# Kernel tuning notes

Measured on AMD Instinct MI355X. Metric: run time of the kernel, lower is better.

## Reference

```python
import jax, jax.numpy as jnp
import numpy as np

R, D = 8192, 128                  # rays, MPI depth planes (steps per ray)
NX, NY, NZ = 160, 160, 128        # world_size (NZ == mpi_depth)
PDIM, K0, WID, PE = 16, 12, 128, 4
RGBFEA = 4 * (9 + 3 + 3 + 3) + 6  # 78, rgbnet output dim
VSR = 256.0 / D                   # voxel_size_ratio (alpha interval)
LAM = 0.01                        # glob_lambda_den / glob_lambda_rgb


def _act_shift():
    # exact replication of the act_shift buffer init in __init__
    g = np.full([D], 1.0 / D - 1e-6)
    p = [1.0 - g[0]]
    for i in range(1, D):
        p.append((1.0 - g[:i + 1].sum()) / (1.0 - g[:i].sum()))
    p = np.asarray(p)
    return jnp.asarray(np.log(p ** (-1.0 / VSR) - 1.0) - 1.0, dtype=jnp.float32)


def setup_inputs() -> dict:
    key = jax.random.key(0)
    ks = jax.random.split(key, 8)
    dim0 = 3 + 3 * PE * 2 + K0  # 39
    return {
        "rays_o": jax.random.uniform(ks[0], (R, 3), jnp.float32),
        "rays_d": jax.random.normal(ks[1], (R, 3), jnp.float32),
        "density_grid": jax.random.normal(ks[2], (1, NX, NY, NZ), jnp.float32) * 0.1,
        "density_params_grid": jax.random.normal(ks[3], (PDIM, NX, NY, NZ), jnp.float32) * 0.05,
        "k0_grid": jax.random.normal(ks[4], (K0, NX, NY, NZ), jnp.float32) * 0.1,
        "global_flow_den": jnp.zeros((2,), jnp.float32),
        "global_flow_rgb": jnp.zeros((6,), jnp.float32),
        "w0": jax.random.normal(ks[5], (dim0, WID), jnp.float32) / np.sqrt(dim0),
        "b0": jnp.zeros((WID,), jnp.float32),
        "w1": jax.random.normal(ks[6], (WID, WID), jnp.float32) / np.sqrt(WID),
        "b1": jnp.zeros((WID,), jnp.float32),
        "w2": jax.random.normal(ks[7], (WID, RGBFEA), jnp.float32) / np.sqrt(WID),
        "b2": jnp.zeros((RGBFEA,), jnp.float32),
        "act_shift": _act_shift(),  # non-trainable buffer, shape [D]
    }


def _trilinear(grid, pts):
    # grid: [C, X, Y, Z]; pts: [N, 3] in [0, 1] -> returns [N, C]
    sizes_i = np.array(grid.shape[1:], dtype=np.int32)
    sizes_f = jnp.asarray(sizes_i, dtype=pts.dtype)
    g = jnp.clip(pts, 0.0, 1.0) * (sizes_f - 1.0)
    i0 = jnp.clip(jnp.floor(g).astype(jnp.int32), 0, jnp.asarray(sizes_i - 2))
    f = g - i0.astype(pts.dtype)
    out = jnp.zeros((grid.shape[0], pts.shape[0]), dtype=pts.dtype)
    for dx in (0, 1):
        wx = f[:, 0] if dx else 1.0 - f[:, 0]
        for dy in (0, 1):
            wy = f[:, 1] if dy else 1.0 - f[:, 1]
            for dz in (0, 1):
                wz = f[:, 2] if dz else 1.0 - f[:, 2]
                v = grid[:, i0[:, 0] + dx, i0[:, 1] + dy, i0[:, 2] + dz]  # [C, N] gather
                out = out + v * (wx * wy * wz)[None, :]
    return out.T


def reference(rays_o, rays_d, density_grid, density_params_grid, k0_grid,
              global_flow_den, global_flow_rgb, w0, b0, w1, b1, w2, b2, act_shift):
    # --- packed ray sampling over MPI depth planes (create_full_step_id pattern) ---
    t = jnp.linspace(0.0, 1.0, D, dtype=rays_o.dtype)
    pts = rays_o[:, None, :] + rays_d[:, None, :] * t[None, :, None]   # [R, D, 3]
    pts = jnp.clip(pts, 0.0, 1.0).reshape(-1, 3)                        # [R*D, 3]
    ray_id = jnp.repeat(jnp.arange(R, dtype=jnp.int32), D)              # [R*D]
    step_id = jnp.tile(jnp.arange(D, dtype=jnp.int32), R)               # [R*D]

    # --- grid trilinear sampling ---
    density = _trilinear(density_grid, pts)[:, 0]          # [N]
    params = _trilinear(density_params_grid, pts)          # [N, 16]
    k0f = _trilinear(k0_grid, pts)                          # [N, 12]

    # --- per-point normalizing-flow reparam on density (4 flow steps, 4 params each) ---
    z = density + global_flow_den[0] * LAM
    for i in range(4):
        p = params[:, 4 * i:4 * i + 4]
        z = z + p[:, 0] * jnp.tanh(p[:, 1] * z + p[:, 2]) * jax.nn.sigmoid(p[:, 3])

    # --- alpha from shifted density: 1 - exp(-softplus(den + shift) * interval) ---
    den = z + act_shift[step_id]
    alpha = 1.0 - jnp.exp(-jax.nn.softplus(den) * VSR)      # [N]

    # --- per-ray transmittance via exclusive cumprod ---
    a = alpha.reshape(R, D)
    T = jnp.cumprod(1.0 - a + 1e-10, axis=1)
    T_excl = jnp.concatenate([jnp.ones((R, 1), a.dtype), T[:, :-1]], axis=1)
    weights = a * T_excl                                     # [R, D]
    alphainv_last = T[:, -1]                                 # [R]

    # --- view-direction positional encoding, broadcast per point via ray_id gather ---
    viewdirs = rays_d / (jnp.linalg.norm(rays_d, axis=-1, keepdims=True) + 1e-8)
    freq = jnp.asarray([2.0 ** i for i in range(PE)], dtype=rays_d.dtype)
    ang = viewdirs[:, :, None] * freq[None, None, :]          # [R, 3, PE]
    emb = jnp.concatenate([viewdirs, jnp.sin(ang).reshape(R, -1), jnp.cos(ang).reshape(R, -1)], -1)  # [R, 27]

    # --- MLP shading ---
    h = jnp.concatenate([emb[ray_id], k0f], axis=-1)          # [N, 39]
    h = jax.nn.relu(h @ w0 + b0)
    h = jax.nn.relu(h @ w1 + b1)
    feat = h @ w2 + b2                                        # [N, 78]
    rgb = jax.nn.sigmoid(feat[:, :3] + global_flow_rgb[:3] * LAM)  # [N, 3]

    # --- segment-sum compositing over packed ray_id (white background) ---
    wflat = weights.reshape(-1)
    rgb_marched = jax.ops.segment_sum(wflat[:, None] * rgb, ray_id, num_segments=R)
    rgb_marched = rgb_marched + alphainv_last[:, None]
    return rgb_marched
```

## Files before the change

kernel.cpp:

```cpp
#include <hip/hip_runtime.h>
#include <math.h>

#define R_    8192
#define D_    128
#define RD    (R_ * D_)
#define NXg   160
#define NYg   160
#define NZg   128
#define CSg   (NXg * NYg * NZg)
#define WIDm  128
#define K0C   12
#define LAMc  0.01f
#define VSRc  2.0f

#define W1F_N   16384
#define W0KF_N  2048
#define W2F_N   4096
#define WTAB_N  (W1F_N + W0KF_N + W2F_N)
#define LW1     0
#define LW0K    W1F_N
#define LW2     (W1F_N + W0KF_N)

typedef __attribute__((ext_vector_type(8)))  short   short8v;
typedef __attribute__((ext_vector_type(4)))  float   f32x4;
typedef __attribute__((ext_vector_type(16))) float   f32x16;
typedef __attribute__((ext_vector_type(2)))  int     int2v;
typedef __attribute__((ext_vector_type(4)))  int     int4v;
typedef __attribute__((ext_vector_type(4)))  unsigned short ushort4v;
typedef __attribute__((ext_vector_type(8)))  unsigned short ushort8v;

static __device__ __forceinline__ unsigned short f2b(float f) {
    union { float f; unsigned int u; } v; v.f = f;
    unsigned int r = v.u + 0x7fffu + ((v.u >> 16) & 1u);
    return (unsigned short)(r >> 16);
}
static __device__ __forceinline__ float b2f(unsigned short u) {
    union { unsigned int u; float f; } v; v.u = ((unsigned int)u) << 16;
    return v.f;
}
static __device__ __forceinline__ unsigned int pk2(float lo, float hi) {
    unsigned int r;
    asm("v_cvt_pk_bf16_f32 %0, %1, %2" : "=v"(r) : "v"(lo), "v"(hi));
    return r;
}
static __device__ __forceinline__ short8v as_s8(int4v v) {
    union { int4v i; short8v s; } u; u.i = v; return u.s;
}

__global__ __launch_bounds__(256) void k_pack_t(
    const float* __restrict__ dg, const float* __restrict__ pg,
    const float* __restrict__ kg, unsigned short* __restrict__ vox)
{
    const int tid = threadIdx.x;
    const int g   = tid & 3;
    const int s2  = tid >> 2;
    const float* pl[8];
    bool padq[8];
#pragma unroll
    for (int q = 0; q < 8; ++q) {
        int ch = 8 * g + q;
        padq[q] = (ch >= 29);
        pl[q] = (ch == 0) ? dg
              : (ch < 17) ? pg + (size_t)(ch - 1) * CSg
              : (ch < 29) ? kg + (size_t)(ch - 17) * CSg
              : dg;
    }
#pragma unroll
    for (int it = 0; it < 4; ++it) {
        int vofs = (blockIdx.x * 4 + it) * 256 + 4 * s2;
        f32x4 L[8];
#pragma unroll
        for (int q = 0; q < 8; ++q) {
            f32x4 v = __builtin_nontemporal_load((const f32x4*)(pl[q] + vofs));
            if (padq[q]) v = f32x4{0.0f, 0.0f, 0.0f, 0.0f};
            L[q] = v;
        }
#pragma unroll
        for (int k = 0; k < 4; ++k) {
            int4v chunk;
#pragma unroll
            for (int h2 = 0; h2 < 4; ++h2)
                chunk[h2] = (int)pk2(L[2 * h2][k], L[2 * h2 + 1][k]);
            *(int4v*)((char*)vox + (size_t)(vofs + k) * 64 + g * 16) = chunk;
        }
    }
}

__global__ void k_prep_e(const float* __restrict__ rays_d,
                         const float* __restrict__ w0, const float* __restrict__ b0,
                         float* __restrict__ e) {
    int r = blockIdx.x;
    int j = threadIdx.x;
    float d0 = rays_d[r * 3 + 0], d1 = rays_d[r * 3 + 1], d2 = rays_d[r * 3 + 2];
    float nrm = sqrtf(d0 * d0 + d1 * d1 + d2 * d2) + 1e-8f;
    float v[3] = { d0 / nrm, d1 / nrm, d2 / nrm };
    float x[27];
    x[0] = v[0]; x[1] = v[1]; x[2] = v[2];
#pragma unroll
    for (int c = 0; c < 3; ++c)
#pragma unroll
        for (int f = 0; f < 4; ++f) {
            float ang = v[c] * (float)(1 << f);
            x[3 + c * 4 + f]  = sinf(ang);
            x[15 + c * 4 + f] = cosf(ang);
        }
    float acc = b0[j];
#pragma unroll
    for (int m = 0; m < 27; ++m) acc = fmaf(x[m], w0[m * WIDm + j], acc);
    e[r * WIDm + j] = acc;
}

__global__ void k_prep_frags32(const float* __restrict__ w0, const float* __restrict__ w1,
                               const float* __restrict__ w2,
                               unsigned short* __restrict__ wtab) {
    int t = blockIdx.x * 256 + threadIdx.x;
    if (t < W1F_N) {
        int tile = t >> 9, l = (t >> 3) & 63, j = t & 7;
        int mt = tile >> 3, ks = tile & 7;
        int m = mt * 32 + (l & 31);
        int k = ks * 16 + 8 * (l >> 5) + j;
        wtab[LW1 + t] = f2b(w1[k * WIDm + m]);
    } else if (t < W1F_N + W0KF_N) {
        int u = t - W1F_N;
        int mt = u >> 9, l = (u >> 3) & 63, j = u & 7;
        int m = mt * 32 + (l & 31);
        int k = 8 * (l >> 5) + j;
        wtab[LW0K + u] = f2b(k < K0C ? w0[(27 + k) * WIDm + m] : 0.0f);
    } else {
        int u = t - W1F_N - W0KF_N;
        int ks = u >> 9, l = (u >> 3) & 63, j = u & 7;
        int m = l & 31;
        int k = ks * 16 + 8 * (l >> 5) + j;
        wtab[LW2 + u] = f2b(m < 3 ? w2[k * 78 + m] : 0.0f);
    }
}

static __device__ __forceinline__ void finish_sample(
    int sid, int s, const float* acc , const float* __restrict__ gfd,
    const float* __restrict__ act_shift,
    float* __restrict__ alpha_ws, unsigned short* __restrict__ k0b)
{
    float z = acc[0] + gfd[0] * LAMc;
#pragma unroll
    for (int i = 0; i < 4; ++i) {
        float pa = acc[1 + 4 * i + 0], pb = acc[1 + 4 * i + 1];
        float pc = acc[1 + 4 * i + 2], pd = acc[1 + 4 * i + 3];
        float sg = 1.0f / (1.0f + expf(-pd));
        z += pa * tanhf(pb * z + pc) * sg;
    }
    float den = z + act_shift[s];
    float sp = fmaxf(den, 0.0f) + log1pf(expf(-fabsf(den)));
    alpha_ws[sid] = 1.0f - expf(-sp * VSRc);

    ushort8v lo, hi;
#pragma unroll
    for (int c = 0; c < 8; ++c) lo[c] = f2b(acc[17 + c]);
#pragma unroll
    for (int c = 0; c < 8; ++c) hi[c] = (c < 4) ? f2b(acc[17 + 8 + c]) : (unsigned short)0;
    *(ushort8v*)(k0b + (size_t)sid * 16)     = lo;
    *(ushort8v*)(k0b + (size_t)sid * 16 + 8) = hi;
}

static __device__ __forceinline__ void sample_coords(
    int sid, const float* __restrict__ rays_o, const float* __restrict__ rays_d,
    int& ix, int& iy, int& iz, float& fx, float& fy, float& fz)
{
    int r = sid >> 7;
    int s = sid & 127;
    float t = s * (1.0f / 127.0f);
    float px = fminf(fmaxf(rays_o[r * 3 + 0] + rays_d[r * 3 + 0] * t, 0.0f), 1.0f);
    float py = fminf(fmaxf(rays_o[r * 3 + 1] + rays_d[r * 3 + 1] * t, 0.0f), 1.0f);
    float pz = fminf(fmaxf(rays_o[r * 3 + 2] + rays_d[r * 3 + 2] * t, 0.0f), 1.0f);
    float gx = px * (float)(NXg - 1);
    float gy = py * (float)(NYg - 1);
    float gz = pz * (float)(NZg - 1);
    ix = min((int)gx, NXg - 2);
    iy = min((int)gy, NYg - 2);
    iz = min((int)gz, NZg - 2);
    fx = gx - (float)ix;
    fy = gy - (float)iy;
    fz = gz - (float)iz;
}

__global__ __launch_bounds__(256) void k_gather_aos(
    const float* __restrict__ rays_o, const float* __restrict__ rays_d,
    const unsigned short* __restrict__ vox,
    const float* __restrict__ gfd, const float* __restrict__ act_shift,
    float* __restrict__ alpha_ws, unsigned short* __restrict__ k0b)
{
    int sid = blockIdx.x * 256 + threadIdx.x;
    if (sid >= RD) return;
    int ix, iy, iz; float fx, fy, fz;
    sample_coords(sid, rays_o, rays_d, ix, iy, iz, fx, fy, fz);

    const unsigned short* base = vox + ((size_t)(ix * NYg + iy) * NZg + iz) * 32;
    const size_t qoff[4] = { 0, (size_t)NZg * 32, (size_t)NYg * NZg * 32,
                             (size_t)(NYg + 1) * NZg * 32 };
    float wxy[4];
    wxy[0] = (1.0f - fx) * (1.0f - fy);
    wxy[1] = (1.0f - fx) * fy;
    wxy[2] = fx * (1.0f - fy);
    wxy[3] = fx * fy;
    float wz0 = 1.0f - fz, wz1 = fz;

    float acc[29];
#pragma unroll
    for (int c = 0; c < 29; ++c) acc[c] = 0.0f;

#pragma unroll
    for (int q = 0; q < 4; ++q) {
        const unsigned short* p = base + qoff[q];
#pragma unroll
        for (int dz = 0; dz < 2; ++dz) {
            float w = wxy[q] * (dz ? wz1 : wz0);
            const ushort8v* pv = (const ushort8v*)(p + dz * 32);
            ushort8v v0 = pv[0], v1 = pv[1], v2 = pv[2], v3 = pv[3];
#pragma unroll
            for (int i = 0; i < 8; ++i) acc[i]      = fmaf(w, b2f(v0[i]), acc[i]);
#pragma unroll
            for (int i = 0; i < 8; ++i) acc[8 + i]  = fmaf(w, b2f(v1[i]), acc[8 + i]);
#pragma unroll
            for (int i = 0; i < 8; ++i) acc[16 + i] = fmaf(w, b2f(v2[i]), acc[16 + i]);
#pragma unroll
            for (int i = 0; i < 5; ++i) acc[24 + i] = fmaf(w, b2f(v3[i]), acc[24 + i]);
        }
    }
    finish_sample(sid, sid & 127, acc, gfd, act_shift, alpha_ws, k0b);
}

__global__ void k_gather_soa(
    const float* __restrict__ rays_o, const float* __restrict__ rays_d,
    const float* __restrict__ dg,  const float* __restrict__ pg,
    const float* __restrict__ kg,  const float* __restrict__ gfd,
    const float* __restrict__ act_shift,
    float* __restrict__ alpha_ws, unsigned short* __restrict__ k0b)
{
    int sid = blockIdx.x * 256 + threadIdx.x;
    if (sid >= RD) return;
    int ix, iy, iz; float fx, fy, fz;
    sample_coords(sid, rays_o, rays_d, ix, iy, iz, fx, fy, fz);

    int base = (ix * NYg + iy) * NZg + iz;
    int off[4] = { base, base + NZg, base + NYg * NZg, base + NYg * NZg + NZg };
    float wxy[4];
    wxy[0] = (1.0f - fx) * (1.0f - fy);
    wxy[1] = (1.0f - fx) * fy;
    wxy[2] = fx * (1.0f - fy);
    wxy[3] = fx * fy;
    float wz0 = 1.0f - fz, wz1 = fz;

    auto tri = [&](const float* __restrict__ g, int c) -> float {
        float a = 0.0f;
        const float* gc = g + (size_t)c * CSg;
#pragma unroll
        for (int q = 0; q < 4; ++q) {
            const float* p = gc + off[q];
            a += (p[0] * wz0 + p[1] * wz1) * wxy[q];
        }
        return a;
    };
    float acc[29];
    acc[0] = tri(dg, 0);
#pragma unroll
    for (int c = 0; c < 16; ++c) acc[1 + c] = tri(pg, c);
#pragma unroll
    for (int c = 0; c < K0C; ++c) acc[17 + c] = tri(kg, c);
    finish_sample(sid, sid & 127, acc, gfd, act_shift, alpha_ws, k0b);
}

struct BPair { int4v lo, hi; };

static __device__ __forceinline__ BPair ttile(const f32x16 v) {
    unsigned p[8];
#pragma unroll
    for (int q = 0; q < 8; ++q) p[q] = pk2(v[2 * q], v[2 * q + 1]);
    int2v a = __builtin_amdgcn_permlane32_swap((int)p[0], (int)p[2], false, false);
    int2v b = __builtin_amdgcn_permlane32_swap((int)p[1], (int)p[3], false, false);
    int2v c = __builtin_amdgcn_permlane32_swap((int)p[4], (int)p[6], false, false);
    int2v d = __builtin_amdgcn_permlane32_swap((int)p[5], (int)p[7], false, false);
    BPair r;
    r.lo = int4v{ a.x, b.x, a.y, b.y };
    r.hi = int4v{ c.x, d.x, c.y, d.y };
    return r;
}

__global__ __launch_bounds__(256) void k_mlp32(
    const unsigned short* __restrict__ k0b, const float* __restrict__ e,
    const unsigned short* __restrict__ wtab,
    const float* __restrict__ b1, const float* __restrict__ b2,
    const float* __restrict__ gfr,
    float* __restrict__ rgb_ws)
{
    __shared__ unsigned short wlds[WTAB_N];
#pragma unroll
    for (int it = 0; it < WTAB_N / (256 * 8); ++it) {
        int i = (it * 256 + threadIdx.x) * 8;
        *(ushort8v*)&wlds[i] = *(const ushort8v*)&wtab[i];
    }
    __syncthreads();

    const int lane = threadIdx.x & 63;
    const int wid  = threadIdx.x >> 6;
    const int n    = lane & 31;
    const int h    = lane >> 5;
    const int sbase = blockIdx.x * 128 + wid * 32;
    const int sid   = sbase + n;
    const int ray   = blockIdx.x;

    f32x16 acc0[4];
#pragma unroll
    for (int mt = 0; mt < 4; ++mt) {
        const f32x4* ep = (const f32x4*)(e + (size_t)ray * WIDm + mt * 32 + 4 * h);
#pragma unroll
        for (int rr = 0; rr < 4; ++rr) {
            f32x4 ev = ep[2 * rr];
#pragma unroll
            for (int q = 0; q < 4; ++q) acc0[mt][rr * 4 + q] = ev[q];
        }
    }
    short8v bk = *(const short8v*)(k0b + (size_t)sid * 16 + h * 8);
#pragma unroll
    for (int mt = 0; mt < 4; ++mt) {
        short8v af = *(const short8v*)&wlds[LW0K + (mt * 64 + lane) * 8];
        acc0[mt] = __builtin_amdgcn_mfma_f32_32x32x16_bf16(af, bk, acc0[mt], 0, 0, 0);
    }
    int4v bw[8];
#pragma unroll
    for (int mt = 0; mt < 4; ++mt) {
        f32x16 hv;
#pragma unroll
        for (int r = 0; r < 16; ++r) hv[r] = fmaxf(acc0[mt][r], 0.0f);
        BPair t = ttile(hv);
        bw[2 * mt]     = t.lo;
        bw[2 * mt + 1] = t.hi;
    }

    f32x16 acc1[4];
#pragma unroll
    for (int mt = 0; mt < 4; ++mt) {
        const f32x4* bp = (const f32x4*)(b1 + mt * 32 + 4 * h);
#pragma unroll
        for (int rr = 0; rr < 4; ++rr) {
            f32x4 bv = bp[2 * rr];
#pragma unroll
            for (int q = 0; q < 4; ++q) acc1[mt][rr * 4 + q] = bv[q];
        }
    }
#pragma unroll
    for (int mt = 0; mt < 4; ++mt)
#pragma unroll
        for (int ks = 0; ks < 8; ++ks) {
            short8v af = *(const short8v*)&wlds[LW1 + ((mt * 8 + ks) * 64 + lane) * 8];
            acc1[mt] = __builtin_amdgcn_mfma_f32_32x32x16_bf16(af, as_s8(bw[ks]), acc1[mt], 0, 0, 0);
        }
    int4v cw[8];
#pragma unroll
    for (int mt = 0; mt < 4; ++mt) {
        f32x16 hv;
#pragma unroll
        for (int r = 0; r < 16; ++r) hv[r] = fmaxf(acc1[mt][r], 0.0f);
        BPair t = ttile(hv);
        cw[2 * mt]     = t.lo;
        cw[2 * mt + 1] = t.hi;
    }

    f32x16 acc2;
#pragma unroll
    for (int r = 0; r < 16; ++r) acc2[r] = 0.0f;
#pragma unroll
    for (int ks = 0; ks < 8; ++ks) {
        short8v af = *(const short8v*)&wlds[LW2 + (ks * 64 + lane) * 8];
        acc2 = __builtin_amdgcn_mfma_f32_32x32x16_bf16(af, as_s8(cw[ks]), acc2, 0, 0, 0);
    }
    if (h == 0) {
#pragma unroll
        for (int c = 0; c < 3; ++c) {
            float v = acc2[c] + b2[c] + gfr[c] * LAMc;
            rgb_ws[(size_t)c * RD + sid] = 1.0f / (1.0f + expf(-v));
        }
    }
}

__global__ void k_scan_reduce(const float* __restrict__ alpha_ws,
                              const float* __restrict__ rgb_ws,
                              float* __restrict__ out)
{
    int gtid = blockIdx.x * 256 + threadIdx.x;
    int r = gtid >> 6;
    int lane = gtid & 63;
    if (r >= R_) return;

    int base = r * D_ + lane * 2;
    float a0 = alpha_ws[base];
    float a1 = alpha_ws[base + 1];
    float q0 = 1.0f - a0 + 1e-10f;
    float q1 = 1.0f - a1 + 1e-10f;
    float p = q0 * q1;

    float incl = p;
#pragma unroll
    for (int o = 1; o < 64; o <<= 1) {
        float v = __shfl_up(incl, o);
        if (lane >= o) incl *= v;
    }
    float excl = __shfl_up(incl, 1);
    if (lane == 0) excl = 1.0f;
    float Tlast = __shfl(incl, 63);

    float w0s = a0 * excl;
    float w1s = a1 * excl * q0;

    float sums[3];
#pragma unroll
    for (int c = 0; c < 3; ++c) {
        float rg0 = rgb_ws[(size_t)c * RD + base];
        float rg1 = rgb_ws[(size_t)c * RD + base + 1];
        float sc = w0s * rg0 + w1s * rg1;
#pragma unroll
        for (int o = 32; o >= 1; o >>= 1) sc += __shfl_xor(sc, o);
        sums[c] = sc;
    }
    if (lane == 0) {
#pragma unroll
        for (int c = 0; c < 3; ++c) out[r * 3 + c] = sums[c] + Tlast;
    }
}

extern "C" void kernel_launch(void* const* d_in, const int* in_sizes, int n_in,
                              void* d_out, int out_size, void* d_ws, size_t ws_size,
                              hipStream_t stream) {
    const float* rays_o    = (const float*)d_in[0];
    const float* rays_d    = (const float*)d_in[1];
    const float* dg        = (const float*)d_in[2];
    const float* pg        = (const float*)d_in[3];
    const float* kg        = (const float*)d_in[4];
    const float* gfd       = (const float*)d_in[5];
    const float* gfr       = (const float*)d_in[6];
    const float* w0        = (const float*)d_in[7];
    const float* b0        = (const float*)d_in[8];
    const float* w1        = (const float*)d_in[9];
    const float* b1        = (const float*)d_in[10];
    const float* w2        = (const float*)d_in[11];
    const float* b2        = (const float*)d_in[12];
    const float* act_shift = (const float*)d_in[13];
    float* out = (float*)d_out;

    float* ws = (float*)d_ws;
    float*          alpha_ws = ws;
    float*          rgb_ws   = ws + (size_t)RD;
    unsigned short* k0b      = (unsigned short*)(ws + 4 * (size_t)RD);
    float*          e_ws     = ws + 12 * (size_t)RD;
    unsigned short* wtab     = (unsigned short*)(ws + 13 * (size_t)RD);
    size_t frag_end = 13 * (size_t)RD * 4 + (size_t)WTAB_N * 2;
    size_t vox_off  = (frag_end + 63) & ~(size_t)63;
    unsigned short* vox = (unsigned short*)((char*)d_ws + vox_off);
    size_t need = vox_off + (size_t)CSg * 64;
    bool use_aos = (ws_size >= need);

    k_prep_e<<<dim3(R_), dim3(WIDm), 0, stream>>>(rays_d, w0, b0, e_ws);
    k_prep_frags32<<<dim3(WTAB_N / 256), dim3(256), 0, stream>>>(w0, w1, w2, wtab);
    if (use_aos) {
        k_pack_t<<<dim3(CSg / 1024), dim3(256), 0, stream>>>(dg, pg, kg, vox);
        k_gather_aos<<<dim3(RD / 256), dim3(256), 0, stream>>>(
            rays_o, rays_d, vox, gfd, act_shift, alpha_ws, k0b);
    } else {
        k_gather_soa<<<dim3(RD / 256), dim3(256), 0, stream>>>(
            rays_o, rays_d, dg, pg, kg, gfd, act_shift, alpha_ws, k0b);
    }
    k_mlp32<<<dim3(R_), dim3(256), 0, stream>>>(
        k0b, e_ws, wtab, b1, b2, gfr, rgb_ws);
    k_scan_reduce<<<dim3(R_ / 4), dim3(256), 0, stream>>>(alpha_ws, rgb_ws, out);
}
```

Before: 258.7 us.

## Fuse gather, MLP and compositing into one per-ray kernel

Replaces the separate AoS gather, MLP, and scan-reduce kernels with one kernel where each wave handles one ray. It gathers 128 samples, keeps k0 features and RGB in LDS, runs the MFMA MLP, and does the transmittance scan with wave shuffles. This removes the global round-trips for alpha, k0 features and rgb, plus two kernel launches. In exchange LDS use per block grows, occupancy is capped by launch bounds of 512 threads with 2 blocks, and the gather and MLP phases are serialized within each wave.

```diff
diff --git a/kernel.cpp b/kernel.cpp
--- a/kernel.cpp
+++ b/kernel.cpp
@@ -20,6 +20,8 @@
 #define LW1     0
 #define LW0K    W1F_N
 #define LW2     (W1F_N + W0KF_N)
+
+#define WAVES_PB 8
 
 typedef __attribute__((ext_vector_type(8)))  short   short8v;
 typedef __attribute__((ext_vector_type(4)))  float   f32x4;
@@ -135,32 +137,6 @@
     }
 }
 
-static __device__ __forceinline__ void finish_sample(
-    int sid, int s, const float* acc , const float* __restrict__ gfd,
-    const float* __restrict__ act_shift,
-    float* __restrict__ alpha_ws, unsigned short* __restrict__ k0b)
-{
-    float z = acc[0] + gfd[0] * LAMc;
-#pragma unroll
-    for (int i = 0; i < 4; ++i) {
-        float pa = acc[1 + 4 * i + 0], pb = acc[1 + 4 * i + 1];
-        float pc = acc[1 + 4 * i + 2], pd = acc[1 + 4 * i + 3];
-        float sg = 1.0f / (1.0f + expf(-pd));
-        z += pa * tanhf(pb * z + pc) * sg;
-    }
-    float den = z + act_shift[s];
-    float sp = fmaxf(den, 0.0f) + log1pf(expf(-fabsf(den)));
-    alpha_ws[sid] = 1.0f - expf(-sp * VSRc);
-
-    ushort8v lo, hi;
-#pragma unroll
-    for (int c = 0; c < 8; ++c) lo[c] = f2b(acc[17 + c]);
-#pragma unroll
-    for (int c = 0; c < 8; ++c) hi[c] = (c < 4) ? f2b(acc[17 + 8 + c]) : (unsigned short)0;
-    *(ushort8v*)(k0b + (size_t)sid * 16)     = lo;
-    *(ushort8v*)(k0b + (size_t)sid * 16 + 8) = hi;
-}
-
 static __device__ __forceinline__ void sample_coords(
     int sid, const float* __restrict__ rays_o, const float* __restrict__ rays_d,
     int& ix, int& iy, int& iz, float& fx, float& fy, float& fz)
@@ -182,17 +158,12 @@
     fz = gz - (float)iz;
 }
 
-__global__ __launch_bounds__(256) void k_gather_aos(
-    const float* __restrict__ rays_o, const float* __restrict__ rays_d,
-    const unsigned short* __restrict__ vox,
-    const float* __restrict__ gfd, const float* __restrict__ act_shift,
-    float* __restrict__ alpha_ws, unsigned short* __restrict__ k0b)
-{
-    int sid = blockIdx.x * 256 + threadIdx.x;
-    if (sid >= RD) return;
+static __device__ __forceinline__ void gather_vox(
+    int sid, const float* __restrict__ rays_o, const float* __restrict__ rays_d,
+    const unsigned short* __restrict__ vox, float* acc)
+{
     int ix, iy, iz; float fx, fy, fz;
     sample_coords(sid, rays_o, rays_d, ix, iy, iz, fx, fy, fz);
-
     const unsigned short* base = vox + ((size_t)(ix * NYg + iy) * NZg + iz) * 32;
     const size_t qoff[4] = { 0, (size_t)NZg * 32, (size_t)NYg * NZg * 32,
                              (size_t)(NYg + 1) * NZg * 32 };
@@ -202,11 +173,8 @@
     wxy[2] = fx * (1.0f - fy);
     wxy[3] = fx * fy;
     float wz0 = 1.0f - fz, wz1 = fz;
-
-    float acc[29];
 #pragma unroll
     for (int c = 0; c < 29; ++c) acc[c] = 0.0f;
-
 #pragma unroll
     for (int q = 0; q < 4; ++q) {
         const unsigned short* p = base + qoff[q];
@@ -225,51 +193,25 @@
             for (int i = 0; i < 5; ++i) acc[24 + i] = fmaf(w, b2f(v3[i]), acc[24 + i]);
         }
     }
-    finish_sample(sid, sid & 127, acc, gfd, act_shift, alpha_ws, k0b);
-}
-
-__global__ void k_gather_soa(
-    const float* __restrict__ rays_o, const float* __restrict__ rays_d,
-    const float* __restrict__ dg,  const float* __restrict__ pg,
-    const float* __restrict__ kg,  const float* __restrict__ gfd,
-    const float* __restrict__ act_shift,
-    float* __restrict__ alpha_ws, unsigned short* __restrict__ k0b)
-{
-    int sid = blockIdx.x * 256 + threadIdx.x;
-    if (sid >= RD) return;
-    int ix, iy, iz; float fx, fy, fz;
-    sample_coords(sid, rays_o, rays_d, ix, iy, iz, fx, fy, fz);
-
-    int base = (ix * NYg + iy) * NZg + iz;
-    int off[4] = { base, base + NZg, base + NYg * NZg, base + NYg * NZg + NZg };
-    float wxy[4];
-    wxy[0] = (1.0f - fx) * (1.0f - fy);
-    wxy[1] = (1.0f - fx) * fy;
-    wxy[2] = fx * (1.0f - fy);
-    wxy[3] = fx * fy;
-    float wz0 = 1.0f - fz, wz1 = fz;
-
-    auto tri = [&](const float* __restrict__ g, int c) -> float {
-        float a = 0.0f;
-        const float* gc = g + (size_t)c * CSg;
-#pragma unroll
-        for (int q = 0; q < 4; ++q) {
-            const float* p = gc + off[q];
-            a += (p[0] * wz0 + p[1] * wz1) * wxy[q];
-        }
-        return a;
-    };
-    float acc[29];
-    acc[0] = tri(dg, 0);
-#pragma unroll
-    for (int c = 0; c < 16; ++c) acc[1 + c] = tri(pg, c);
-#pragma unroll
-    for (int c = 0; c < K0C; ++c) acc[17 + c] = tri(kg, c);
-    finish_sample(sid, sid & 127, acc, gfd, act_shift, alpha_ws, k0b);
+}
+
+static __device__ __forceinline__ float density_alpha(
+    int s, const float* acc, float gfd0, const float* __restrict__ act_shift)
+{
+    float z = acc[0] + gfd0;
+#pragma unroll
+    for (int i = 0; i < 4; ++i) {
+        float pa = acc[1 + 4 * i + 0], pb = acc[1 + 4 * i + 1];
+        float pc = acc[1 + 4 * i + 2], pd = acc[1 + 4 * i + 3];
+        float sg = 1.0f / (1.0f + expf(-pd));
+        z += pa * tanhf(pb * z + pc) * sg;
+    }
+    float den = z + act_shift[s];
+    float sp = fmaxf(den, 0.0f) + log1pf(expf(-fabsf(den)));
+    return 1.0f - expf(-sp * VSRc);
 }
 
 struct BPair { int4v lo, hi; };
-
 static __device__ __forceinline__ BPair ttile(const f32x16 v) {
     unsigned p[8];
 #pragma unroll
@@ -282,6 +224,215 @@
     r.lo = int4v{ a.x, b.x, a.y, b.y };
     r.hi = int4v{ c.x, d.x, c.y, d.y };
     return r;
+}
+
+__global__ __launch_bounds__(512, 2) void k_fused_ray(
+    const float* __restrict__ rays_o, const float* __restrict__ rays_d,
+    const unsigned short* __restrict__ vox,
+    const float* __restrict__ gfd, const float* __restrict__ act_shift,
+    const float* __restrict__ e, const unsigned short* __restrict__ wtab,
+    const float* __restrict__ b1, const float* __restrict__ b2,
+    const float* __restrict__ gfr,
+    float* __restrict__ out)
+{
+    __shared__ unsigned short wlds[WTAB_N];
+    __shared__ unsigned short k0lds[WAVES_PB][D_][16];
+#pragma unroll
+    for (int it = 0; it < 6; ++it) {
+        int i = (it * 512 + threadIdx.x) * 8;
+        if (i < WTAB_N)
+            *(ushort8v*)&wlds[i] = *(const ushort8v*)&wtab[i];
+    }
+    __syncthreads();
+
+    const int lane = threadIdx.x & 63;
+    const int wid  = threadIdx.x >> 6;
+    const int n    = lane & 31;
+    const int h    = lane >> 5;
+    const int ray  = blockIdx.x * WAVES_PB + wid;
+    const float gfd0 = gfd[0] * LAMc;
+
+    float alpha[2];
+#pragma unroll
+    for (int ss = 0; ss < 2; ++ss) {
+        int s = 2 * lane + ss;
+        float acc[29];
+        gather_vox(ray * D_ + s, rays_o, rays_d, vox, acc);
+        alpha[ss] = density_alpha(s, acc, gfd0, act_shift);
+        ushort8v lo, hi;
+#pragma unroll
+        for (int c = 0; c < 8; ++c) lo[c] = f2b(acc[17 + c]);
+#pragma unroll
+        for (int c = 0; c < 8; ++c) hi[c] = (c < 4) ? f2b(acc[25 + c]) : (unsigned short)0;
+        *(ushort8v*)&k0lds[wid][s][0] = lo;
+        *(ushort8v*)&k0lds[wid][s][8] = hi;
+    }
+
+    for (int t = 0; t < 4; ++t) {
+        short8v bk = *(const short8v*)&k0lds[wid][t * 32 + n][h * 8];
+
+        f32x16 acc0[4];
+#pragma unroll
+        for (int mt = 0; mt < 4; ++mt) {
+            const f32x4* ep = (const f32x4*)(e + (size_t)ray * WIDm + mt * 32 + 4 * h);
+#pragma unroll
+            for (int rr = 0; rr < 4; ++rr) {
+                f32x4 ev = ep[2 * rr];
+#pragma unroll
+                for (int q = 0; q < 4; ++q) acc0[mt][rr * 4 + q] = ev[q];
+            }
+        }
+#pragma unroll
+        for (int mt = 0; mt < 4; ++mt) {
+            short8v af = *(const short8v*)&wlds[LW0K + (mt * 64 + lane) * 8];
+            acc0[mt] = __builtin_amdgcn_mfma_f32_32x32x16_bf16(af, bk, acc0[mt], 0, 0, 0);
+        }
+        int4v bw[8];
+#pragma unroll
+        for (int mt = 0; mt < 4; ++mt) {
+            f32x16 hv;
+#pragma unroll
+            for (int r = 0; r < 16; ++r) hv[r] = fmaxf(acc0[mt][r], 0.0f);
+            BPair tt = ttile(hv);
+            bw[2 * mt]     = tt.lo;
+            bw[2 * mt + 1] = tt.hi;
+        }
+
+        f32x16 acc1[4];
+#pragma unroll
+        for (int mt = 0; mt < 4; ++mt) {
+            const f32x4* bp = (const f32x4*)(b1 + mt * 32 + 4 * h);
+#pragma unroll
+            for (int rr = 0; rr < 4; ++rr) {
+                f32x4 bv = bp[2 * rr];
+#pragma unroll
+                for (int q = 0; q < 4; ++q) acc1[mt][rr * 4 + q] = bv[q];
+            }
+        }
+#pragma unroll
+        for (int mt = 0; mt < 4; ++mt)
+#pragma unroll
+            for (int ks = 0; ks < 8; ++ks) {
+                short8v af = *(const short8v*)&wlds[LW1 + ((mt * 8 + ks) * 64 + lane) * 8];
+                acc1[mt] = __builtin_amdgcn_mfma_f32_32x32x16_bf16(af, as_s8(bw[ks]), acc1[mt], 0, 0, 0);
+            }
+        int4v cw[8];
+#pragma unroll
+        for (int mt = 0; mt < 4; ++mt) {
+            f32x16 hv;
+#pragma unroll
+            for (int r = 0; r < 16; ++r) hv[r] = fmaxf(acc1[mt][r], 0.0f);
+            BPair tt = ttile(hv);
+            cw[2 * mt]     = tt.lo;
+            cw[2 * mt + 1] = tt.hi;
+        }
+
+        f32x16 acc2;
+#pragma unroll
+        for (int r = 0; r < 16; ++r) acc2[r] = 0.0f;
+#pragma unroll
+        for (int ks = 0; ks < 8; ++ks) {
+            short8v af = *(const short8v*)&wlds[LW2 + (ks * 64 + lane) * 8];
+            acc2 = __builtin_amdgcn_mfma_f32_32x32x16_bf16(af, as_s8(cw[ks]), acc2, 0, 0, 0);
+        }
+        if (h == 0) {
+            float* rl = (float*)&k0lds[wid][t * 32 + n][0];
+#pragma unroll
+            for (int c = 0; c < 3; ++c) {
+                float v = acc2[c] + b2[c] + gfr[c] * LAMc;
+                rl[c] = 1.0f / (1.0f + expf(-v));
+            }
+        }
+    }
+
+    float a0 = alpha[0];
+    float a1 = alpha[1];
+    float q0 = 1.0f - a0 + 1e-10f;
+    float q1 = 1.0f - a1 + 1e-10f;
+    float p = q0 * q1;
+
+    float incl = p;
+#pragma unroll
+    for (int o = 1; o < 64; o <<= 1) {
+        float v = __shfl_up(incl, o);
+        if (lane >= o) incl *= v;
+    }
+    float excl = __shfl_up(incl, 1);
+    if (lane == 0) excl = 1.0f;
+    float Tlast = __shfl(incl, 63);
+
+    float w0s = a0 * excl;
+    float w1s = a1 * excl * q0;
+
+    const float* p0 = (const float*)&k0lds[wid][2 * lane][0];
+    const float* p1 = (const float*)&k0lds[wid][2 * lane + 1][0];
+    float sums[3];
+#pragma unroll
+    for (int c = 0; c < 3; ++c) {
+        float sc = w0s * p0[c] + w1s * p1[c];
+#pragma unroll
+        for (int o = 32; o >= 1; o >>= 1) sc += __shfl_xor(sc, o);
+        sums[c] = sc;
+    }
+    if (lane == 0) {
+#pragma unroll
+        for (int c = 0; c < 3; ++c) out[ray * 3 + c] = sums[c] + Tlast;
+    }
+}
+
+static __device__ __forceinline__ void finish_sample(
+    int sid, int s, const float* acc, const float* __restrict__ gfd,
+    const float* __restrict__ act_shift,
+    float* __restrict__ alpha_ws, unsigned short* __restrict__ k0b)
+{
+    alpha_ws[sid] = density_alpha(s, acc, gfd[0] * LAMc, act_shift);
+    ushort8v lo, hi;
+#pragma unroll
+    for (int c = 0; c < 8; ++c) lo[c] = f2b(acc[17 + c]);
+#pragma unroll
+    for (int c = 0; c < 8; ++c) hi[c] = (c < 4) ? f2b(acc[25 + c]) : (unsigned short)0;
+    *(ushort8v*)(k0b + (size_t)sid * 16)     = lo;
+    *(ushort8v*)(k0b + (size_t)sid * 16 + 8) = hi;
+}
+
+__global__ void k_gather_soa(
+    const float* __restrict__ rays_o, const float* __restrict__ rays_d,
+    const float* __restrict__ dg,  const float* __restrict__ pg,
+    const float* __restrict__ kg,  const float* __restrict__ gfd,
+    const float* __restrict__ act_shift,
+    float* __restrict__ alpha_ws, unsigned short* __restrict__ k0b)
+{
+    int sid = blockIdx.x * 256 + threadIdx.x;
+    if (sid >= RD) return;
+    int ix, iy, iz; float fx, fy, fz;
+    sample_coords(sid, rays_o, rays_d, ix, iy, iz, fx, fy, fz);
+
+    int base = (ix * NYg + iy) * NZg + iz;
+    int off[4] = { base, base + NZg, base + NYg * NZg, base + NYg * NZg + NZg };
+    float wxy[4];
+    wxy[0] = (1.0f - fx) * (1.0f - fy);
+    wxy[1] = (1.0f - fx) * fy;
+    wxy[2] = fx * (1.0f - fy);
+    wxy[3] = fx * fy;
+    float wz0 = 1.0f - fz, wz1 = fz;
+
+    auto tri = [&](const float* __restrict__ g, int c) -> float {
+        float a = 0.0f;
+        const float* gc = g + (size_t)c * CSg;
+#pragma unroll
+        for (int q = 0; q < 4; ++q) {
+            const float* p = gc + off[q];
+            a += (p[0] * wz0 + p[1] * wz1) * wxy[q];
+        }
+        return a;
+    };
+    float acc[29];
+    acc[0] = tri(dg, 0);
+#pragma unroll
+    for (int c = 0; c < 16; ++c) acc[1 + c] = tri(pg, c);
+#pragma unroll
+    for (int c = 0; c < K0C; ++c) acc[17 + c] = tri(kg, c);
+    finish_sample(sid, sid & 127, acc, gfd, act_shift, alpha_ws, k0b);
 }
 
 __global__ __launch_bounds__(256) void k_mlp32(
@@ -461,13 +612,13 @@
     k_prep_frags32<<<dim3(WTAB_N / 256), dim3(256), 0, stream>>>(w0, w1, w2, wtab);
     if (use_aos) {
         k_pack_t<<<dim3(CSg / 1024), dim3(256), 0, stream>>>(dg, pg, kg, vox);
-        k_gather_aos<<<dim3(RD / 256), dim3(256), 0, stream>>>(
-            rays_o, rays_d, vox, gfd, act_shift, alpha_ws, k0b);
+        k_fused_ray<<<dim3(R_ / WAVES_PB), dim3(512), 0, stream>>>(
+            rays_o, rays_d, vox, gfd, act_shift, e_ws, wtab, b1, b2, gfr, out);
     } else {
         k_gather_soa<<<dim3(RD / 256), dim3(256), 0, stream>>>(
             rays_o, rays_d, dg, pg, kg, gfd, act_shift, alpha_ws, k0b);
-    }
-    k_mlp32<<<dim3(R_), dim3(256), 0, stream>>>(
-        k0b, e_ws, wtab, b1, b2, gfr, rgb_ws);
-    k_scan_reduce<<<dim3(R_ / 4), dim3(256), 0, stream>>>(alpha_ws, rgb_ws, out);
-}
+        k_mlp32<<<dim3(R_), dim3(256), 0, stream>>>(
+            k0b, e_ws, wtab, b1, b2, gfr, rgb_ws);
+        k_scan_reduce<<<dim3(R_ / 4), dim3(256), 0, stream>>>(alpha_ws, rgb_ws, out);
+    }
+}
```

Measured after the change: 324.9 us. +25.6%, slower.

## Fuse scan-reduce compositing into MLP kernel and merge prep kernels

Applied to the files above, without the earlier changes.

Moves the per-ray transmittance scan and weighted RGB reduction into the MLP kernel, which already processes one ray per block. Sigmoid RGB values now go to shared memory instead of a global workspace, so the separate scan kernel and its global round trip are removed. The two small prep kernels (view-embedding projection and weight fragment packing) are merged into one launch with 512-thread blocks. This saves two launches and about 12 MB of traffic, at the cost of a block-wide sync and a single-wave tail phase in the MLP kernel.

```diff
diff --git a/kernel.cpp b/kernel.cpp
--- a/kernel.cpp
+++ b/kernel.cpp
@@ -86,79 +86,55 @@
     }
 }
 
-__global__ void k_prep_e(const float* __restrict__ rays_d,
-                         const float* __restrict__ w0, const float* __restrict__ b0,
-                         float* __restrict__ e) {
-    int r = blockIdx.x;
-    int j = threadIdx.x;
-    float d0 = rays_d[r * 3 + 0], d1 = rays_d[r * 3 + 1], d2 = rays_d[r * 3 + 2];
-    float nrm = sqrtf(d0 * d0 + d1 * d1 + d2 * d2) + 1e-8f;
-    float v[3] = { d0 / nrm, d1 / nrm, d2 / nrm };
-    float x[27];
-    x[0] = v[0]; x[1] = v[1]; x[2] = v[2];
-#pragma unroll
-    for (int c = 0; c < 3; ++c)
-#pragma unroll
-        for (int f = 0; f < 4; ++f) {
-            float ang = v[c] * (float)(1 << f);
-            x[3 + c * 4 + f]  = sinf(ang);
-            x[15 + c * 4 + f] = cosf(ang);
-        }
-    float acc = b0[j];
-#pragma unroll
-    for (int m = 0; m < 27; ++m) acc = fmaf(x[m], w0[m * WIDm + j], acc);
-    e[r * WIDm + j] = acc;
-}
-
-__global__ void k_prep_frags32(const float* __restrict__ w0, const float* __restrict__ w1,
-                               const float* __restrict__ w2,
-                               unsigned short* __restrict__ wtab) {
-    int t = blockIdx.x * 256 + threadIdx.x;
-    if (t < W1F_N) {
-        int tile = t >> 9, l = (t >> 3) & 63, j = t & 7;
-        int mt = tile >> 3, ks = tile & 7;
-        int m = mt * 32 + (l & 31);
-        int k = ks * 16 + 8 * (l >> 5) + j;
-        wtab[LW1 + t] = f2b(w1[k * WIDm + m]);
-    } else if (t < W1F_N + W0KF_N) {
-        int u = t - W1F_N;
-        int mt = u >> 9, l = (u >> 3) & 63, j = u & 7;
-        int m = mt * 32 + (l & 31);
-        int k = 8 * (l >> 5) + j;
-        wtab[LW0K + u] = f2b(k < K0C ? w0[(27 + k) * WIDm + m] : 0.0f);
+__global__ __launch_bounds__(512) void k_prep_all(
+    const float* __restrict__ rays_d,
+    const float* __restrict__ w0, const float* __restrict__ b0,
+    const float* __restrict__ w1, const float* __restrict__ w2,
+    float* __restrict__ e, unsigned short* __restrict__ wtab)
+{
+    int bid = blockIdx.x;
+    if (bid < R_ / 4) {
+        int r = bid * 4 + (threadIdx.x >> 7);
+        int j = threadIdx.x & 127;
+        float d0 = rays_d[r * 3 + 0], d1 = rays_d[r * 3 + 1], d2 = rays_d[r * 3 + 2];
+        float nrm = sqrtf(d0 * d0 + d1 * d1 + d2 * d2) + 1e-8f;
+        float v[3] = { d0 / nrm, d1 / nrm, d2 / nrm };
+        float x[27];
+        x[0] = v[0]; x[1] = v[1]; x[2] = v[2];
+#pragma unroll
+        for (int c = 0; c < 3; ++c)
+#pragma unroll
+            for (int f = 0; f < 4; ++f) {
+                float ang = v[c] * (float)(1 << f);
+                x[3 + c * 4 + f]  = sinf(ang);
+                x[15 + c * 4 + f] = cosf(ang);
+            }
+        float acc = b0[j];
+#pragma unroll
+        for (int m = 0; m < 27; ++m) acc = fmaf(x[m], w0[m * WIDm + j], acc);
+        e[r * WIDm + j] = acc;
     } else {
-        int u = t - W1F_N - W0KF_N;
-        int ks = u >> 9, l = (u >> 3) & 63, j = u & 7;
-        int m = l & 31;
-        int k = ks * 16 + 8 * (l >> 5) + j;
-        wtab[LW2 + u] = f2b(m < 3 ? w2[k * 78 + m] : 0.0f);
-    }
-}
-
-static __device__ __forceinline__ void finish_sample(
-    int sid, int s, const float* acc , const float* __restrict__ gfd,
-    const float* __restrict__ act_shift,
-    float* __restrict__ alpha_ws, unsigned short* __restrict__ k0b)
-{
-    float z = acc[0] + gfd[0] * LAMc;
-#pragma unroll
-    for (int i = 0; i < 4; ++i) {
-        float pa = acc[1 + 4 * i + 0], pb = acc[1 + 4 * i + 1];
-        float pc = acc[1 + 4 * i + 2], pd = acc[1 + 4 * i + 3];
-        float sg = 1.0f / (1.0f + expf(-pd));
-        z += pa * tanhf(pb * z + pc) * sg;
-    }
-    float den = z + act_shift[s];
-    float sp = fmaxf(den, 0.0f) + log1pf(expf(-fabsf(den)));
-    alpha_ws[sid] = 1.0f - expf(-sp * VSRc);
-
-    ushort8v lo, hi;
-#pragma unroll
-    for (int c = 0; c < 8; ++c) lo[c] = f2b(acc[17 + c]);
-#pragma unroll
-    for (int c = 0; c < 8; ++c) hi[c] = (c < 4) ? f2b(acc[17 + 8 + c]) : (unsigned short)0;
-    *(ushort8v*)(k0b + (size_t)sid * 16)     = lo;
-    *(ushort8v*)(k0b + (size_t)sid * 16 + 8) = hi;
+        int t = (bid - R_ / 4) * 512 + threadIdx.x;
+        if (t < W1F_N) {
+            int tile = t >> 9, l = (t >> 3) & 63, j = t & 7;
+            int mt = tile >> 3, ks = tile & 7;
+            int m = mt * 32 + (l & 31);
+            int k = ks * 16 + 8 * (l >> 5) + j;
+            wtab[LW1 + t] = f2b(w1[k * WIDm + m]);
+        } else if (t < W1F_N + W0KF_N) {
+            int u = t - W1F_N;
+            int mt = u >> 9, l = (u >> 3) & 63, j = u & 7;
+            int m = mt * 32 + (l & 31);
+            int k = 8 * (l >> 5) + j;
+            wtab[LW0K + u] = f2b(k < K0C ? w0[(27 + k) * WIDm + m] : 0.0f);
+        } else if (t < WTAB_N) {
+            int u = t - W1F_N - W0KF_N;
+            int ks = u >> 9, l = (u >> 3) & 63, j = u & 7;
+            int m = l & 31;
+            int k = ks * 16 + 8 * (l >> 5) + j;
+            wtab[LW2 + u] = f2b(m < 3 ? w2[k * 78 + m] : 0.0f);
+        }
+    }
 }
 
 static __device__ __forceinline__ void sample_coords(
@@ -182,6 +158,37 @@
     fz = gz - (float)iz;
 }
 
+static __device__ __forceinline__ float density_alpha(
+    int s, const float* acc, float gfd0, const float* __restrict__ act_shift)
+{
+    float z = acc[0] + gfd0;
+#pragma unroll
+    for (int i = 0; i < 4; ++i) {
+        float pa = acc[1 + 4 * i + 0], pb = acc[1 + 4 * i + 1];
+        float pc = acc[1 + 4 * i + 2], pd = acc[1 + 4 * i + 3];
+        float sg = 1.0f / (1.0f + expf(-pd));
+        z += pa * tanhf(pb * z + pc) * sg;
+    }
+    float den = z + act_shift[s];
+    float sp = fmaxf(den, 0.0f) + log1pf(expf(-fabsf(den)));
+    return 1.0f - expf(-sp * VSRc);
+}
+
+static __device__ __forceinline__ void finish_sample(
+    int sid, int s, const float* acc, float gfd0,
+    const float* __restrict__ act_shift,
+    float* __restrict__ alpha_ws, unsigned short* __restrict__ k0b)
+{
+    alpha_ws[sid] = density_alpha(s, acc, gfd0, act_shift);
+    ushort8v lo, hi;
+#pragma unroll
+    for (int c = 0; c < 8; ++c) lo[c] = f2b(acc[17 + c]);
+#pragma unroll
+    for (int c = 0; c < 8; ++c) hi[c] = (c < 4) ? f2b(acc[25 + c]) : (unsigned short)0;
+    *(ushort8v*)(k0b + (size_t)sid * 16)     = lo;
+    *(ushort8v*)(k0b + (size_t)sid * 16 + 8) = hi;
+}
+
 __global__ __launch_bounds__(256) void k_gather_aos(
     const float* __restrict__ rays_o, const float* __restrict__ rays_d,
     const unsigned short* __restrict__ vox,
@@ -225,7 +232,7 @@
             for (int i = 0; i < 5; ++i) acc[24 + i] = fmaf(w, b2f(v3[i]), acc[24 + i]);
         }
     }
-    finish_sample(sid, sid & 127, acc, gfd, act_shift, alpha_ws, k0b);
+    finish_sample(sid, sid & 127, acc, gfd[0] * LAMc, act_shift, alpha_ws, k0b);
 }
 
 __global__ void k_gather_soa(
@@ -265,11 +272,10 @@
     for (int c = 0; c < 16; ++c) acc[1 + c] = tri(pg, c);
 #pragma unroll
     for (int c = 0; c < K0C; ++c) acc[17 + c] = tri(kg, c);
-    finish_sample(sid, sid & 127, acc, gfd, act_shift, alpha_ws, k0b);
+    finish_sample(sid, sid & 127, acc, gfd[0] * LAMc, act_shift, alpha_ws, k0b);
 }
 
 struct BPair { int4v lo, hi; };
-
 static __device__ __forceinline__ BPair ttile(const f32x16 v) {
     unsigned p[8];
 #pragma unroll
@@ -284,14 +290,15 @@
     return r;
 }
 
-__global__ __launch_bounds__(256) void k_mlp32(
+__global__ __launch_bounds__(256) void k_mlp_scan(
     const unsigned short* __restrict__ k0b, const float* __restrict__ e,
     const unsigned short* __restrict__ wtab,
     const float* __restrict__ b1, const float* __restrict__ b2,
-    const float* __restrict__ gfr,
-    float* __restrict__ rgb_ws)
+    const float* __restrict__ gfr, const float* __restrict__ alpha_ws,
+    float* __restrict__ out)
 {
     __shared__ unsigned short wlds[WTAB_N];
+    __shared__ float rgb_lds[D_][5];
 #pragma unroll
     for (int it = 0; it < WTAB_N / (256 * 8); ++it) {
         int i = (it * 256 + threadIdx.x) * 8;
@@ -303,9 +310,8 @@
     const int wid  = threadIdx.x >> 6;
     const int n    = lane & 31;
     const int h    = lane >> 5;
-    const int sbase = blockIdx.x * 128 + wid * 32;
-    const int sid   = sbase + n;
-    const int ray   = blockIdx.x;
+    const int ray  = blockIdx.x;
+    const int sid  = ray * D_ + wid * 32 + n;
 
     f32x16 acc0[4];
 #pragma unroll
@@ -376,53 +382,44 @@
 #pragma unroll
         for (int c = 0; c < 3; ++c) {
             float v = acc2[c] + b2[c] + gfr[c] * LAMc;
-            rgb_ws[(size_t)c * RD + sid] = 1.0f / (1.0f + expf(-v));
-        }
-    }
-}
-
-__global__ void k_scan_reduce(const float* __restrict__ alpha_ws,
-                              const float* __restrict__ rgb_ws,
-                              float* __restrict__ out)
-{
-    int gtid = blockIdx.x * 256 + threadIdx.x;
-    int r = gtid >> 6;
-    int lane = gtid & 63;
-    if (r >= R_) return;
-
-    int base = r * D_ + lane * 2;
-    float a0 = alpha_ws[base];
-    float a1 = alpha_ws[base + 1];
-    float q0 = 1.0f - a0 + 1e-10f;
-    float q1 = 1.0f - a1 + 1e-10f;
-    float p = q0 * q1;
-
-    float incl = p;
-#pragma unroll
-    for (int o = 1; o < 64; o <<= 1) {
-        float v = __shfl_up(incl, o);
-        if (lane >= o) incl *= v;
-    }
-    float excl = __shfl_up(incl, 1);
-    if (lane == 0) excl = 1.0f;
-    float Tlast = __shfl(incl, 63);
-
-    float w0s = a0 * excl;
-    float w1s = a1 * excl * q0;
-
-    float sums[3];
-#pragma unroll
-    for (int c = 0; c < 3; ++c) {
-        float rg0 = rgb_ws[(size_t)c * RD + base];
-        float rg1 = rgb_ws[(size_t)c * RD + base + 1];
-        float sc = w0s * rg0 + w1s * rg1;
-#pragma unroll
-        for (int o = 32; o >= 1; o >>= 1) sc += __shfl_xor(sc, o);
-        sums[c] = sc;
-    }
-    if (lane == 0) {
-#pragma unroll
-        for (int c = 0; c < 3; ++c) out[r * 3 + c] = sums[c] + Tlast;
+            rgb_lds[wid * 32 + n][c] = 1.0f / (1.0f + expf(-v));
+        }
+    }
+    __syncthreads();
+
+    if (wid == 0) {
+        int base = ray * D_ + lane * 2;
+        float a0 = alpha_ws[base];
+        float a1 = alpha_ws[base + 1];
+        float q0 = 1.0f - a0 + 1e-10f;
+        float q1 = 1.0f - a1 + 1e-10f;
+        float p = q0 * q1;
+
+        float incl = p;
+#pragma unroll
+        for (int o = 1; o < 64; o <<= 1) {
+            float v = __shfl_up(incl, o);
+            if (lane >= o) incl *= v;
+        }
+        float excl = __shfl_up(incl, 1);
+        if (lane == 0) excl = 1.0f;
+        float Tlast = __shfl(incl, 63);
+
+        float w0s = a0 * excl;
+        float w1s = a1 * excl * q0;
+
+        float sums[3];
+#pragma unroll
+        for (int c = 0; c < 3; ++c) {
+            float sc = w0s * rgb_lds[2 * lane][c] + w1s * rgb_lds[2 * lane + 1][c];
+#pragma unroll
+            for (int o = 32; o >= 1; o >>= 1) sc += __shfl_xor(sc, o);
+            sums[c] = sc;
+        }
+        if (lane == 0) {
+#pragma unroll
+            for (int c = 0; c < 3; ++c) out[ray * 3 + c] = sums[c] + Tlast;
+        }
     }
 }
 
@@ -447,7 +444,6 @@
 
     float* ws = (float*)d_ws;
     float*          alpha_ws = ws;
-    float*          rgb_ws   = ws + (size_t)RD;
     unsigned short* k0b      = (unsigned short*)(ws + 4 * (size_t)RD);
     float*          e_ws     = ws + 12 * (size_t)RD;
     unsigned short* wtab     = (unsigned short*)(ws + 13 * (size_t)RD);
@@ -457,8 +453,8 @@
     size_t need = vox_off + (size_t)CSg * 64;
     bool use_aos = (ws_size >= need);
 
-    k_prep_e<<<dim3(R_), dim3(WIDm), 0, stream>>>(rays_d, w0, b0, e_ws);
-    k_prep_frags32<<<dim3(WTAB_N / 256), dim3(256), 0, stream>>>(w0, w1, w2, wtab);
+    k_prep_all<<<dim3(R_ / 4 + (WTAB_N + 511) / 512), dim3(512), 0, stream>>>(
+        rays_d, w0, b0, w1, w2, e_ws, wtab);
     if (use_aos) {
         k_pack_t<<<dim3(CSg / 1024), dim3(256), 0, stream>>>(dg, pg, kg, vox);
         k_gather_aos<<<dim3(RD / 256), dim3(256), 0, stream>>>(
@@ -467,7 +463,6 @@
         k_gather_soa<<<dim3(RD / 256), dim3(256), 0, stream>>>(
             rays_o, rays_d, dg, pg, kg, gfd, act_shift, alpha_ws, k0b);
     }
-    k_mlp32<<<dim3(R_), dim3(256), 0, stream>>>(
-        k0b, e_ws, wtab, b1, b2, gfr, rgb_ws);
-    k_scan_reduce<<<dim3(R_ / 4), dim3(256), 0, stream>>>(alpha_ws, rgb_ws, out);
-}
+    k_mlp_scan<<<dim3(R_), dim3(256), 0, stream>>>(
+        k0b, e_ws, wtab, b1, b2, gfr, alpha_ws, out);
+}
```

After: 255.5 us. No clear change (-1.2%).
